# Kernel optimization log

Hardware: AMD Instinct MI355X
Metric: run time of the kernel (lower is better)

Reference implementation:

```python
import jax, jax.numpy as jnp
import numpy as np

N_PAPER, N_AUTHOR, N_SUBJECT = 100000, 50000, 5000
N_INP, N_HID, N_OUT = 256, 128, 16
E_PA, E_AP, E_PS, E_SP = 600000, 600000, 200000, 200000


def _seg_mean(msg, dst, n_dst):
    # segment-sum over destination nodes, normalized by in-degree (mean agg)
    s = jax.ops.segment_sum(msg, dst, num_segments=n_dst)
    deg = jax.ops.segment_sum(jnp.ones((dst.shape[0],), msg.dtype), dst, num_segments=n_dst)
    return s / jnp.maximum(deg, 1.0)[:, None]


def _rel_conv(x_src, w, src, dst, n_dst):
    # transform-then-gather (fewer FLOPs than gather-then-transform)
    m = (x_src @ w)[src]  # [E, n_hid]
    return _seg_mean(m, dst, n_dst)


def setup_inputs() -> dict:
    key = jax.random.key(0)
    ks = jax.random.split(key, 32)
    s = 0.05
    inp = {
        'x_paper': jax.random.normal(ks[0], (N_PAPER, N_INP), jnp.float32),
        'x_author': jax.random.normal(ks[1], (N_AUTHOR, N_INP), jnp.float32),
        'x_subject': jax.random.normal(ks[2], (N_SUBJECT, N_INP), jnp.float32),
        'pa_src': jax.random.randint(ks[3], (E_PA,), 0, N_PAPER),
        'pa_dst': jax.random.randint(ks[4], (E_PA,), 0, N_AUTHOR),
        'ap_src': jax.random.randint(ks[5], (E_AP,), 0, N_AUTHOR),
        'ap_dst': jax.random.randint(ks[6], (E_AP,), 0, N_PAPER),
        'ps_src': jax.random.randint(ks[7], (E_PS,), 0, N_PAPER),
        'ps_dst': jax.random.randint(ks[8], (E_PS,), 0, N_SUBJECT),
        'sp_src': jax.random.randint(ks[9], (E_SP,), 0, N_SUBJECT),
        'sp_dst': jax.random.randint(ks[10], (E_SP,), 0, N_PAPER),
        # HeteroAdaptMLP params (per node type, n_layer=1, gelu)
        'enc_w_paper': jax.random.normal(ks[11], (N_INP, N_HID), jnp.float32) * s,
        'enc_b_paper': jnp.zeros((N_HID,), jnp.float32),
        'enc_w_author': jax.random.normal(ks[12], (N_INP, N_HID), jnp.float32) * s,
        'enc_b_author': jnp.zeros((N_HID,), jnp.float32),
        'enc_w_subject': jax.random.normal(ks[13], (N_INP, N_HID), jnp.float32) * s,
        'enc_b_subject': jnp.zeros((N_HID,), jnp.float32),
        # per-relation GraphConv weights, 2 layers x 4 relations
        'w0_pa': jax.random.normal(ks[14], (N_HID, N_HID), jnp.float32) * s,
        'w0_ap': jax.random.normal(ks[15], (N_HID, N_HID), jnp.float32) * s,
        'w0_ps': jax.random.normal(ks[16], (N_HID, N_HID), jnp.float32) * s,
        'w0_sp': jax.random.normal(ks[17], (N_HID, N_HID), jnp.float32) * s,
        'w1_pa': jax.random.normal(ks[18], (N_HID, N_HID), jnp.float32) * s,
        'w1_ap': jax.random.normal(ks[19], (N_HID, N_HID), jnp.float32) * s,
        'w1_ps': jax.random.normal(ks[20], (N_HID, N_HID), jnp.float32) * s,
        'w1_sp': jax.random.normal(ks[21], (N_HID, N_HID), jnp.float32) * s,
        # output head
        'out_w': jax.random.normal(ks[22], (N_HID, N_OUT), jnp.float32) * s,
        'out_b': jnp.zeros((N_OUT,), jnp.float32),
    }
    return inp


def reference(x_paper, x_author, x_subject,
              pa_src, pa_dst, ap_src, ap_dst, ps_src, ps_dst, sp_src, sp_dst,
              enc_w_paper, enc_b_paper, enc_w_author, enc_b_author,
              enc_w_subject, enc_b_subject,
              w0_pa, w0_ap, w0_ps, w0_sp, w1_pa, w1_ap, w1_ps, w1_sp,
              out_w, out_b):
    # task_specific_encoder: per-node-type 1-layer MLP with gelu
    h_p = jax.nn.gelu(x_paper @ enc_w_paper + enc_b_paper)
    h_a = jax.nn.gelu(x_author @ enc_w_author + enc_b_author)
    h_s = jax.nn.gelu(x_subject @ enc_w_subject + enc_b_subject)

    for (w_pa, w_ap, w_ps, w_sp) in ((w0_pa, w0_ap, w0_ps, w0_sp),
                                     (w1_pa, w1_ap, w1_ps, w1_sp)):
        # per-relation gather -> GraphConv(mean) -> scatter; 'sum' across relations
        new_a = _rel_conv(h_p, w_pa, pa_src, pa_dst, N_AUTHOR)
        new_s = _rel_conv(h_p, w_ps, ps_src, ps_dst, N_SUBJECT)
        new_p = (_rel_conv(h_a, w_ap, ap_src, ap_dst, N_PAPER)
                 + _rel_conv(h_s, w_sp, sp_src, sp_dst, N_PAPER))
        # activation=None, self_loop=False, dropout is identity at inference
        h_p, h_a, h_s = new_p, new_a, new_s

    # out_key = 'paper'
    return h_p @ out_w + out_b
```

## Files before the change

### kernel.cpp

```cpp
#include <hip/hip_runtime.h>
#include <math.h>

constexpr int NP = 100000, NA = 50000, NS = 5000;
constexpr int EPA = 600000, EAP = 600000, EPS = 200000, ESP = 200000;
constexpr int ETOT = EPA + EPS + EAP + ESP;
constexpr int NT   = NA + NS + NP + NP;
constexpr int OFF_PS = EPA, OFF_AP = EPA + EPS, OFF_SP = EPA + EPS + EAP;
constexpr int ROW_PS = NA, ROW_AP = NA + NS, ROW_SP = NA + NS + NP;

constexpr int NB_FOLD  = 2;
constexpr int NB_PACK  = (256*128)/256;
constexpr int NB_HIST  = (ETOT + 1023)/1024;
constexpr int NB_ENC   = (NP + 63)/64;
constexpr int NB_FILLA = (OFF_AP + 1023)/1024;
constexpr int NB_FILLB = ((ETOT-OFF_AP)+1023)/1024;
constexpr int NB_G16   = ((NA+NS)*16 + 255)/256;

typedef short s16x8 __attribute__((ext_vector_type(8)));
typedef float f32x4 __attribute__((ext_vector_type(4)));
typedef unsigned short u16;

__device__ __forceinline__ float gelu_f(float x) {
  float x3 = x*x*x;
  return 0.5f*x*(1.0f + tanhf(0.7978845608028654f*(x + 0.044715f*x3)));
}
__device__ __forceinline__ u16 f2bf(float f) {
  unsigned u = __float_as_uint(f);
  u += 0x7fffu + ((u >> 16) & 1u);
  return (u16)(u >> 16);
}
__device__ __forceinline__ float bf2f(u16 s) {
  return __uint_as_float((unsigned)s << 16);
}

__global__ __launch_bounds__(256) void fold_pack(
    const float* __restrict__ w0_pa, const float* __restrict__ w1_ap,
    const float* __restrict__ w0_ps, const float* __restrict__ w1_sp,
    const float* __restrict__ out_w, u16* __restrict__ WFb,
    const float* __restrict__ ewp, u16* __restrict__ wpk)
{
  __shared__ float Wst[64*132];
  __shared__ float OW[128*16];
  __shared__ float U[128*16];
  const int b = blockIdx.x, tid = threadIdx.x;

  if (b >= NB_FOLD) {
    int o = (b - NB_FOLD)*256 + tid;
    int bb = o & 7;
    int l  = (o >> 3) & 63;
    int cf = (o >> 9) & 7;
    int ks = o >> 12;
    wpk[o] = f2bf(ewp[(ks*32 + (l>>4)*8 + bb)*128 + cf*16 + (l & 15)]);
    return;
  }

  const float* w0 = (b == 0) ? w0_pa : w0_ps;
  const float* w1 = (b == 0) ? w1_ap : w1_sp;
  for (int i = tid; i < 512; i += 256) ((float4*)OW)[i] = ((const float4*)out_w)[i];
  for (int half = 0; half < 2; ++half) {
    __syncthreads();
    for (int i = tid; i < 64*32; i += 256) {
      int row = i >> 5, q = i & 31;
      float4 v = ((const float4*)(w1 + (size_t)(half*64 + row)*128))[q];
      *(float4*)&Wst[row*132 + q*4] = v;
    }
    __syncthreads();
    #pragma unroll
    for (int i = 0; i < 4; ++i) {
      int idx = tid + 256*i;
      int r = idx >> 4, c = idx & 15;
      float acc = 0.f;
      #pragma unroll 8
      for (int k = 0; k < 128; ++k) acc = fmaf(Wst[r*132+k], OW[k*16+c], acc);
      U[(half*64 + r)*16 + c] = acc;
    }
  }
  for (int half = 0; half < 2; ++half) {
    __syncthreads();
    for (int i = tid; i < 64*32; i += 256) {
      int row = i >> 5, q = i & 31;
      float4 v = ((const float4*)(w0 + (size_t)(half*64 + row)*128))[q];
      *(float4*)&Wst[row*132 + q*4] = v;
    }
    __syncthreads();
    #pragma unroll
    for (int i = 0; i < 4; ++i) {
      int idx = tid + 256*i;
      int r = idx >> 4, c = idx & 15;
      float acc = 0.f;
      #pragma unroll 8
      for (int k = 0; k < 128; ++k) acc = fmaf(Wst[r*132+k], U[k*16+c], acc);
      int k = half*64 + r;
      int ks = k >> 5;
      int lane = (((k >> 3) & 3) << 4) | c;
      WFb[(((size_t)ks*2 + b)*64 + lane)*8 + (k & 7)] = f2bf(acc);
    }
  }
}

__global__ __launch_bounds__(256) void hist_enc(
    const int* __restrict__ pa_d, const int* __restrict__ ps_d,
    const int* __restrict__ ap_d, const int* __restrict__ sp_d,
    int* __restrict__ h, u16* __restrict__ rank16,
    const float* __restrict__ A, const u16* __restrict__ Wp,
    const float* __restrict__ bias, const u16* __restrict__ WFb,
    float* __restrict__ YZ)
{
  __shared__ u16 hl[64][136];
  const int b = blockIdx.x;
  const int tid = threadIdx.x;

  if (!(b & 1)) {
    const int e = (b >> 1)*1024 + tid*4;
    if (e >= ETOT) return;
    const int* dsts; int off;
    if (e < OFF_PS)      { dsts = pa_d;          off = 0; }
    else if (e < OFF_AP) { dsts = ps_d - OFF_PS; off = ROW_PS; }
    else if (e < OFF_SP) { dsts = ap_d - OFF_AP; off = ROW_AP; }
    else                 { dsts = sp_d - OFF_SP; off = ROW_SP; }
    int4 d4 = *(const int4*)(dsts + e);
    unsigned p0 = (unsigned)atomicAdd(&h[off + d4.x], 1);
    unsigned p1 = (unsigned)atomicAdd(&h[off + d4.y], 1);
    unsigned p2 = (unsigned)atomicAdd(&h[off + d4.z], 1);
    unsigned p3 = (unsigned)atomicAdd(&h[off + d4.w], 1);
    uint2 rr;
    rr.x = (p0 & 0xffffu) | (p1 << 16);
    rr.y = (p2 & 0xffffu) | (p3 << 16);
    *(uint2*)(rank16 + e) = rr;
    return;
  }

  const int eb = b >> 1;
  const int lane = tid & 63, wv = tid >> 6;
  const int rowbase = eb*64 + wv*16;
  const int m  = lane & 15;
  const int kq = lane >> 4;

  f32x4 acc[8];
  #pragma unroll
  for (int j = 0; j < 8; ++j) acc[j] = (f32x4){0.f,0.f,0.f,0.f};

  const int r0 = rowbase + m;
  const bool v0 = r0 < NP;
  const float* Arow = A + (size_t)r0*256 + kq*8;

  #pragma unroll
  for (int ks = 0; ks < 8; ++ks) {
    s16x8 a0 = {0,0,0,0,0,0,0,0};
    if (v0) {
      float4 f = *(const float4*)(Arow + ks*32);
      float4 g = *(const float4*)(Arow + ks*32 + 4);
      a0[0]=(short)f2bf(f.x); a0[1]=(short)f2bf(f.y); a0[2]=(short)f2bf(f.z); a0[3]=(short)f2bf(f.w);
      a0[4]=(short)f2bf(g.x); a0[5]=(short)f2bf(g.y); a0[6]=(short)f2bf(g.z); a0[7]=(short)f2bf(g.w);
    }
    const s16x8* Wf = (const s16x8*)Wp + (size_t)ks*512 + lane;
    #pragma unroll
    for (int cf = 0; cf < 8; ++cf)
      acc[cf] = __builtin_amdgcn_mfma_f32_16x16x32_bf16(a0, Wf[cf*64], acc[cf], 0, 0, 0);
  }

  const int rlb = wv*16 + kq*4;
  #pragma unroll
  for (int cf = 0; cf < 8; ++cf) {
    const int col = cf*16 + m;
    const float bcol = bias[col];
    #pragma unroll
    for (int r = 0; r < 4; ++r)
      hl[rlb + r][col] = f2bf(gelu_f(acc[cf][r] + bcol));
  }
  __syncthreads();

  const s16x8* WFv = (const s16x8*)WFb;
  f32x4 yacc[2];
  yacc[0] = (f32x4){0.f,0.f,0.f,0.f};
  yacc[1] = (f32x4){0.f,0.f,0.f,0.f};
  #pragma unroll
  for (int ks = 0; ks < 4; ++ks) {
    s16x8 af = *(const s16x8*)&hl[wv*16 + m][ks*32 + kq*8];
    yacc[0] = __builtin_amdgcn_mfma_f32_16x16x32_bf16(af, WFv[(ks*2+0)*64 + lane], yacc[0], 0, 0, 0);
    yacc[1] = __builtin_amdgcn_mfma_f32_16x16x32_bf16(af, WFv[(ks*2+1)*64 + lane], yacc[1], 0, 0, 0);
  }
  #pragma unroll
  for (int r = 0; r < 4; ++r) {
    const int row = rowbase + kq*4 + r;
    if (row < NP) {
      YZ[(size_t)row*32 + m]      = yacc[0][r];
      YZ[(size_t)row*32 + 16 + m] = yacc[1][r];
    }
  }
}

__global__ __launch_bounds__(256) void scan_partial(const int* __restrict__ in, int n,
                                                    int* __restrict__ part) {
  __shared__ int red[4];
  int base = blockIdx.x*4096;
  int sum = 0;
  for (int i = threadIdx.x; i < 4096; i += 256) {
    int idx = base + i;
    sum += (idx < n) ? in[idx] : 0;
  }
  #pragma unroll
  for (int off = 32; off; off >>= 1) sum += __shfl_down(sum, off, 64);
  if ((threadIdx.x & 63) == 0) red[threadIdx.x >> 6] = sum;
  __syncthreads();
  if (threadIdx.x == 0) part[blockIdx.x] = red[0]+red[1]+red[2]+red[3];
}

__global__ __launch_bounds__(256) void scan_chunk(const int* __restrict__ in, int n,
    const int* __restrict__ part, int* __restrict__ out)
{
  int off0 = 0;
  for (int i = 0; i < (int)blockIdx.x; ++i) off0 += part[i];
  const int base = blockIdx.x*4096 + threadIdx.x*16;
  int loc[16]; int s = 0;
  #pragma unroll
  for (int j = 0; j < 16; ++j) {
    int idx = base + j;
    int v = (idx < n) ? in[idx] : 0;
    loc[j] = s; s += v;
  }
  __shared__ int ts[256];
  ts[threadIdx.x] = s; __syncthreads();
  for (int off = 1; off < 256; off <<= 1) {
    int t = (threadIdx.x >= off) ? ts[threadIdx.x - off] : 0;
    __syncthreads();
    ts[threadIdx.x] += t;
    __syncthreads();
  }
  int excl = off0 + ts[threadIdx.x] - s;
  #pragma unroll
  for (int j = 0; j < 16; ++j) {
    int idx = base + j;
    if (idx < n) out[idx] = excl + loc[j];
    if (idx == n-1) out[n] = excl + loc[j] + in[idx];
  }
}

__device__ __forceinline__ void fill4(int e,
    const int* __restrict__ pa_s, const int* __restrict__ pa_d,
    const int* __restrict__ ps_s, const int* __restrict__ ps_d,
    const int* __restrict__ ap_s, const int* __restrict__ ap_d,
    const int* __restrict__ sp_s, const int* __restrict__ sp_d,
    const int* __restrict__ rp, const u16* __restrict__ rank16,
    int* __restrict__ ci)
{
  const int *srcs, *dsts; int off;
  if (e < OFF_PS)      { srcs = pa_s;          dsts = pa_d;          off = 0; }
  else if (e < OFF_AP) { srcs = ps_s - OFF_PS; dsts = ps_d - OFF_PS; off = ROW_PS; }
  else if (e < OFF_SP) { srcs = ap_s - OFF_AP; dsts = ap_d - OFF_AP; off = ROW_AP; }
  else                 { srcs = sp_s - OFF_SP; dsts = sp_d - OFF_SP; off = ROW_SP; }
  int4 s4 = *(const int4*)(srcs + e);
  int4 d4 = *(const int4*)(dsts + e);
  uint2 rr = *(const uint2*)(rank16 + e);
  ci[rp[off + d4.x] + (int)(rr.x & 0xffffu)] = s4.x;
  ci[rp[off + d4.y] + (int)(rr.x >> 16)]     = s4.y;
  ci[rp[off + d4.z] + (int)(rr.y & 0xffffu)] = s4.z;
  ci[rp[off + d4.w] + (int)(rr.y >> 16)]     = s4.w;
}

__global__ __launch_bounds__(256) void fill_paps(
    const int* __restrict__ pa_s, const int* __restrict__ pa_d,
    const int* __restrict__ ps_s, const int* __restrict__ ps_d,
    const int* __restrict__ ap_s, const int* __restrict__ ap_d,
    const int* __restrict__ sp_s, const int* __restrict__ sp_d,
    const int* __restrict__ rp, const u16* __restrict__ rank16,
    int* __restrict__ ci)
{
  int e = blockIdx.x*1024 + threadIdx.x*4;
  if (e < OFF_AP)
    fill4(e, pa_s, pa_d, ps_s, ps_d, ap_s, ap_d, sp_s, sp_d, rp, rank16, ci);
}

__global__ __launch_bounds__(256) void g16_fill(
    const float* __restrict__ yz,
    const int* __restrict__ rp, const int* __restrict__ ci,
    float* __restrict__ m16,
    const int* __restrict__ pa_s, const int* __restrict__ pa_d,
    const int* __restrict__ ps_s, const int* __restrict__ ps_d,
    const int* __restrict__ ap_s, const int* __restrict__ ap_d,
    const int* __restrict__ sp_s, const int* __restrict__ sp_d,
    const u16* __restrict__ rank16, int* __restrict__ ci_w)
{
  const int b = blockIdx.x;
  if (b < NB_FILLB) {
    int e = OFF_AP + b*1024 + threadIdx.x*4;
    if (e < ETOT)
      fill4(e, pa_s, pa_d, ps_s, ps_d, ap_s, ap_d, sp_s, sp_d, rp, rank16, ci_w);
    return;
  }
  int t = (b - NB_FILLB)*256 + threadIdx.x;
  int row = t >> 4, lane = t & 15;
  if (row >= NA + NS) return;
  int beg = rp[row], end = rp[row+1];
  int off = (row < NA ? 0 : 16) + lane;
  float a = 0.f, bb = 0.f;
  int e = beg;
  for (; e + 1 < end; e += 2) {
    a  += yz[(size_t)ci[e]  *32 + off];
    bb += yz[(size_t)ci[e+1]*32 + off];
  }
  if (e < end) a += yz[(size_t)ci[e]*32 + off];
  int d = end - beg;
  m16[(size_t)row*16 + lane] = (a + bb) / (float)(d > 0 ? d : 1);
}

__global__ __launch_bounds__(256) void gather2_16(
    const float* __restrict__ f1, const int* __restrict__ rp1,
    const float* __restrict__ f2, const int* __restrict__ rp2,
    const int* __restrict__ ci, const float* __restrict__ ob,
    float* __restrict__ O, int n)
{
  int t = blockIdx.x*256 + threadIdx.x;
  int row = t >> 4, lane = t & 15;
  if (row >= n) return;

  float s1 = 0.f, s1b = 0.f;
  {
    int beg = rp1[row], end = rp1[row+1];
    int e = beg;
    for (; e + 1 < end; e += 2) {
      s1  += f1[(size_t)ci[e]  *16 + lane];
      s1b += f1[(size_t)ci[e+1]*16 + lane];
    }
    if (e < end) s1 += f1[(size_t)ci[e]*16 + lane];
    int d = end - beg;
    s1 = (s1 + s1b) / (float)(d > 0 ? d : 1);
  }
  float s2 = 0.f, s2b = 0.f;
  {
    int beg = rp2[row], end = rp2[row+1];
    int e = beg;
    for (; e + 1 < end; e += 2) {
      s2  += f2[(size_t)ci[e]  *16 + lane];
      s2b += f2[(size_t)ci[e+1]*16 + lane];
    }
    if (e < end) s2 += f2[(size_t)ci[e]*16 + lane];
    int d = end - beg;
    s2 = (s2 + s2b) / (float)(d > 0 ? d : 1);
  }
  O[(size_t)row*16 + lane] = s1 + s2 + ob[lane];
}

extern "C" void kernel_launch(void* const* d_in, const int* in_sizes, int n_in,
                              void* d_out, int out_size, void* d_ws, size_t ws_size,
                              hipStream_t stream)
{
  const float* x_p = (const float*)d_in[0];
  const int* pa_src=(const int*)d_in[3]; const int* pa_dst=(const int*)d_in[4];
  const int* ap_src=(const int*)d_in[5]; const int* ap_dst=(const int*)d_in[6];
  const int* ps_src=(const int*)d_in[7]; const int* ps_dst=(const int*)d_in[8];
  const int* sp_src=(const int*)d_in[9]; const int* sp_dst=(const int*)d_in[10];
  const float* ewp=(const float*)d_in[11]; const float* ebp=(const float*)d_in[12];
  const float* w0_pa=(const float*)d_in[17];
  const float* w0_ps=(const float*)d_in[19];
  const float* w1_ap=(const float*)d_in[22];
  const float* w1_sp=(const float*)d_in[24];
  const float* out_w=(const float*)d_in[25]; const float* out_b=(const float*)d_in[26];
  float* out = (float*)d_out;

  char* wp = (char*)d_ws;
  auto alloc = [&](size_t bytes) { char* p = wp; wp += (bytes + 255) & ~(size_t)255; return p; };
  float* yz     = (float*)alloc((size_t)NP*32*4);
  int*   ci     = (int*)alloc((size_t)ETOT*4);
  float* m16    = (float*)alloc((size_t)(NA+NS)*16*4);
  u16*   wpk    = (u16*)alloc((size_t)256*128*2);
  u16*   WFb    = (u16*)alloc((size_t)8*64*8*2);
  int*   h      = (int*)alloc((size_t)NT*4);
  u16*   rank16 = (u16*)alloc((size_t)ETOT*2);
  int*   rpG    = (int*)alloc((size_t)(NT+1)*4);
  int*   part   = (int*)alloc((size_t)64*4);

  hipMemsetAsync(h, 0, (size_t)NT*4, stream);
  fold_pack<<<NB_FOLD+NB_PACK,256,0,stream>>>(
      w0_pa, w1_ap, w0_ps, w1_sp, out_w, WFb, ewp, wpk);

  hist_enc<<<NB_HIST+NB_ENC,256,0,stream>>>(
      pa_dst, ps_dst, ap_dst, sp_dst, h, rank16,
      x_p, wpk, ebp, WFb, yz);

  int nch = (NT + 4095)/4096;
  scan_partial<<<nch,256,0,stream>>>(h, NT, part);
  scan_chunk  <<<nch,256,0,stream>>>(h, NT, part, rpG);

  fill_paps<<<NB_FILLA,256,0,stream>>>(
      pa_src, pa_dst, ps_src, ps_dst, ap_src, ap_dst, sp_src, sp_dst,
      rpG, rank16, ci);

  g16_fill<<<NB_FILLB+NB_G16,256,0,stream>>>(
      yz, rpG, ci, m16,
      pa_src, pa_dst, ps_src, ps_dst, ap_src, ap_dst, sp_src, sp_dst,
      rank16, ci);

  gather2_16<<<(((size_t)NP*16)+255)/256,256,0,stream>>>(
      m16, rpG + ROW_AP,
      m16 + (size_t)NA*16, rpG + ROW_SP,
      ci, out_b, out, NP);
}
```

Before: 200.4 us.

## Split fused histogram/encoder kernel and stage encoder input rows through LDS

The combined histogram+encoder launch, which interleaved blocks of both kinds, is split into two separate kernels. The encoder now loads each 64-row tile of x_paper with coalesced float4 reads into shared memory as bf16, then feeds the MFMA from LDS instead of strided per-lane global reads. This targets poor global-load coalescing in the encoder, at the cost of an extra launch and losing the overlap between atomic-heavy histogram blocks and compute-heavy encoder blocks. It also uses a larger LDS buffer per block, which may reduce occupancy.

```diff
diff --git a/kernel.cpp b/kernel.cpp
--- a/kernel.cpp
+++ b/kernel.cpp
@@ -11,7 +11,6 @@
 constexpr int NB_FOLD  = 2;
 constexpr int NB_PACK  = (256*128)/256;
 constexpr int NB_HIST  = (ETOT + 1023)/1024;
-constexpr int NB_ENC   = (NP + 63)/64;
 constexpr int NB_FILLA = (OFF_AP + 1023)/1024;
 constexpr int NB_FILLB = ((ETOT-OFF_AP)+1023)/1024;
 constexpr int NB_G16   = ((NA+NS)*16 + 255)/256;
@@ -28,9 +27,6 @@
   unsigned u = __float_as_uint(f);
   u += 0x7fffu + ((u >> 16) & 1u);
   return (u16)(u >> 16);
-}
-__device__ __forceinline__ float bf2f(u16 s) {
-  return __uint_as_float((unsigned)s << 16);
 }
 
 __global__ __launch_bounds__(256) void fold_pack(
@@ -98,94 +94,94 @@
   }
 }
 
-__global__ __launch_bounds__(256) void hist_enc(
+__global__ void hist(
     const int* __restrict__ pa_d, const int* __restrict__ ps_d,
     const int* __restrict__ ap_d, const int* __restrict__ sp_d,
-    int* __restrict__ h, u16* __restrict__ rank16,
+    int* __restrict__ h, u16* __restrict__ rank16)
+{
+  const int e = blockIdx.x*1024 + threadIdx.x*4;
+  if (e >= ETOT) return;
+  const int* dsts; int off;
+  if (e < OFF_PS)      { dsts = pa_d;          off = 0; }
+  else if (e < OFF_AP) { dsts = ps_d - OFF_PS; off = ROW_PS; }
+  else if (e < OFF_SP) { dsts = ap_d - OFF_AP; off = ROW_AP; }
+  else                 { dsts = sp_d - OFF_SP; off = ROW_SP; }
+  int4 d4 = *(const int4*)(dsts + e);
+  unsigned p0 = (unsigned)atomicAdd(&h[off + d4.x], 1);
+  unsigned p1 = (unsigned)atomicAdd(&h[off + d4.y], 1);
+  unsigned p2 = (unsigned)atomicAdd(&h[off + d4.z], 1);
+  unsigned p3 = (unsigned)atomicAdd(&h[off + d4.w], 1);
+  uint2 rr;
+  rr.x = (p0 & 0xffffu) | (p1 << 16);
+  rr.y = (p2 & 0xffffu) | (p3 << 16);
+  *(uint2*)(rank16 + e) = rr;
+}
+
+__global__ __launch_bounds__(256) void enc(
     const float* __restrict__ A, const u16* __restrict__ Wp,
     const float* __restrict__ bias, const u16* __restrict__ WFb,
     float* __restrict__ YZ)
 {
-  __shared__ u16 hl[64][136];
-  const int b = blockIdx.x;
+  __shared__ u16 xs[64*264];
   const int tid = threadIdx.x;
-
-  if (!(b & 1)) {
-    const int e = (b >> 1)*1024 + tid*4;
-    if (e >= ETOT) return;
-    const int* dsts; int off;
-    if (e < OFF_PS)      { dsts = pa_d;          off = 0; }
-    else if (e < OFF_AP) { dsts = ps_d - OFF_PS; off = ROW_PS; }
-    else if (e < OFF_SP) { dsts = ap_d - OFF_AP; off = ROW_AP; }
-    else                 { dsts = sp_d - OFF_SP; off = ROW_SP; }
-    int4 d4 = *(const int4*)(dsts + e);
-    unsigned p0 = (unsigned)atomicAdd(&h[off + d4.x], 1);
-    unsigned p1 = (unsigned)atomicAdd(&h[off + d4.y], 1);
-    unsigned p2 = (unsigned)atomicAdd(&h[off + d4.z], 1);
-    unsigned p3 = (unsigned)atomicAdd(&h[off + d4.w], 1);
-    uint2 rr;
-    rr.x = (p0 & 0xffffu) | (p1 << 16);
-    rr.y = (p2 & 0xffffu) | (p3 << 16);
-    *(uint2*)(rank16 + e) = rr;
-    return;
-  }
-
-  const int eb = b >> 1;
+  const int rowbase = blockIdx.x*64;
+
+  #pragma unroll
+  for (int i = 0; i < 16; ++i) {
+    int idx = i*256 + tid;
+    int row = idx >> 6, c4 = idx & 63;
+    int grow = rowbase + row;
+    float4 v = make_float4(0.f,0.f,0.f,0.f);
+    if (grow < NP) v = *(const float4*)(A + (size_t)grow*256 + c4*4);
+    ushort4 bv;
+    bv.x = f2bf(v.x); bv.y = f2bf(v.y); bv.z = f2bf(v.z); bv.w = f2bf(v.w);
+    *(ushort4*)&xs[row*264 + c4*4] = bv;
+  }
+  __syncthreads();
+
   const int lane = tid & 63, wv = tid >> 6;
-  const int rowbase = eb*64 + wv*16;
-  const int m  = lane & 15;
-  const int kq = lane >> 4;
+  const int m = lane & 15, kq = lane >> 4;
+  const int rtile = wv*16;
 
   f32x4 acc[8];
   #pragma unroll
   for (int j = 0; j < 8; ++j) acc[j] = (f32x4){0.f,0.f,0.f,0.f};
 
-  const int r0 = rowbase + m;
-  const bool v0 = r0 < NP;
-  const float* Arow = A + (size_t)r0*256 + kq*8;
-
   #pragma unroll
   for (int ks = 0; ks < 8; ++ks) {
-    s16x8 a0 = {0,0,0,0,0,0,0,0};
-    if (v0) {
-      float4 f = *(const float4*)(Arow + ks*32);
-      float4 g = *(const float4*)(Arow + ks*32 + 4);
-      a0[0]=(short)f2bf(f.x); a0[1]=(short)f2bf(f.y); a0[2]=(short)f2bf(f.z); a0[3]=(short)f2bf(f.w);
-      a0[4]=(short)f2bf(g.x); a0[5]=(short)f2bf(g.y); a0[6]=(short)f2bf(g.z); a0[7]=(short)f2bf(g.w);
-    }
+    s16x8 a0 = *(const s16x8*)&xs[(rtile + m)*264 + ks*32 + kq*8];
     const s16x8* Wf = (const s16x8*)Wp + (size_t)ks*512 + lane;
     #pragma unroll
     for (int cf = 0; cf < 8; ++cf)
       acc[cf] = __builtin_amdgcn_mfma_f32_16x16x32_bf16(a0, Wf[cf*64], acc[cf], 0, 0, 0);
   }
 
-  const int rlb = wv*16 + kq*4;
+  const int rlb = rtile + kq*4;
   #pragma unroll
   for (int cf = 0; cf < 8; ++cf) {
     const int col = cf*16 + m;
     const float bcol = bias[col];
     #pragma unroll
     for (int r = 0; r < 4; ++r)
-      hl[rlb + r][col] = f2bf(gelu_f(acc[cf][r] + bcol));
+      xs[(rlb + r)*264 + col] = f2bf(gelu_f(acc[cf][r] + bcol));
   }
   __syncthreads();
 
   const s16x8* WFv = (const s16x8*)WFb;
-  f32x4 yacc[2];
-  yacc[0] = (f32x4){0.f,0.f,0.f,0.f};
-  yacc[1] = (f32x4){0.f,0.f,0.f,0.f};
+  f32x4 y0 = (f32x4){0.f,0.f,0.f,0.f};
+  f32x4 y1 = (f32x4){0.f,0.f,0.f,0.f};
   #pragma unroll
   for (int ks = 0; ks < 4; ++ks) {
-    s16x8 af = *(const s16x8*)&hl[wv*16 + m][ks*32 + kq*8];
-    yacc[0] = __builtin_amdgcn_mfma_f32_16x16x32_bf16(af, WFv[(ks*2+0)*64 + lane], yacc[0], 0, 0, 0);
-    yacc[1] = __builtin_amdgcn_mfma_f32_16x16x32_bf16(af, WFv[(ks*2+1)*64 + lane], yacc[1], 0, 0, 0);
+    s16x8 af = *(const s16x8*)&xs[(rtile + m)*264 + ks*32 + kq*8];
+    y0 = __builtin_amdgcn_mfma_f32_16x16x32_bf16(af, WFv[(ks*2+0)*64 + lane], y0, 0, 0, 0);
+    y1 = __builtin_amdgcn_mfma_f32_16x16x32_bf16(af, WFv[(ks*2+1)*64 + lane], y1, 0, 0, 0);
   }
   #pragma unroll
   for (int r = 0; r < 4; ++r) {
-    const int row = rowbase + kq*4 + r;
+    const int row = rowbase + rtile + kq*4 + r;
     if (row < NP) {
-      YZ[(size_t)row*32 + m]      = yacc[0][r];
-      YZ[(size_t)row*32 + 16 + m] = yacc[1][r];
+      YZ[(size_t)row*32 + m]      = y0[r];
+      YZ[(size_t)row*32 + 16 + m] = y1[r];
     }
   }
 }
@@ -374,9 +370,9 @@
   fold_pack<<<NB_FOLD+NB_PACK,256,0,stream>>>(
       w0_pa, w1_ap, w0_ps, w1_sp, out_w, WFb, ewp, wpk);
 
-  hist_enc<<<NB_HIST+NB_ENC,256,0,stream>>>(
-      pa_dst, ps_dst, ap_dst, sp_dst, h, rank16,
-      x_p, wpk, ebp, WFb, yz);
+  hist<<<NB_HIST,256,0,stream>>>(pa_dst, ps_dst, ap_dst, sp_dst, h, rank16);
+
+  enc<<<(NP+63)/64,256,0,stream>>>(x_p, wpk, ebp, WFb, yz);
 
   int nch = (NT + 4095)/4096;
   scan_partial<<<nch,256,0,stream>>>(h, NT, part);
```

New measurement: 234.8 us. 17.2% more time.
